# Performance work log

Measured on AMD Instinct MI355X. Metric: run time of the kernel, lower is better.

The kernel has to match this reference:

```python
import jax, jax.numpy as jnp
import numpy as np

IN_FEATURES = 64 * 64 * 3  # 12288, hard-coded in the torch module

# Sign with straight-through estimator (BinaryNet-style): fwd = sign(x),
# bwd = grad * 1{|x| <= 1} (hardtanh clip).
@jax.custom_vjp
def ste_sign(x):
    return jnp.sign(x)

def _ste_fwd(x):
    return jnp.sign(x), x

def _ste_bwd(x, g):
    return (g * (jnp.abs(x) <= 1.0).astype(g.dtype),)

ste_sign.defvjp(_ste_fwd, _ste_bwd)


def setup_inputs() -> dict:
    key = jax.random.key(0)
    k1, k2 = jax.random.split(key)
    B, C = 8192, 1000
    inp = jax.random.normal(k1, (B, IN_FEATURES), dtype=jnp.float32)
    # Linear weight init scale ~ U(-1/sqrt(fan_in), 1/sqrt(fan_in)); use scaled normal
    weight = jax.random.normal(k2, (C, IN_FEATURES), dtype=jnp.float32) * (1.0 / np.sqrt(IN_FEATURES))
    return {"input": inp, "weight": weight}


def reference(input, weight):
    x = input.reshape(-1, IN_FEATURES)
    # F.linear(sign(x), sign(W)) = sign(x) @ sign(W)^T  -> [B, num_classes]
    return jnp.einsum("bd,cd->bc", ste_sign(x), ste_sign(weight))
```

## Files before the change

kernel.cpp:

```cpp
#include <hip/hip_runtime.h>
#include <hip/hip_bf16.h>


#define K_DIM   12288
#define N_CLS   1000
#define N_PAD   1024
#define KSPLIT  4
#define K_QUART (K_DIM / KSPLIT)
#define STAGE_BYTES (N_PAD * 64)
#define N_STAGE_TOT (K_DIM / 64)
#define CHUNK_STAGES 2
#define CHUNK_K  (CHUNK_STAGES * 64)
#define CHUNKS   (K_QUART / CHUNK_K)
#define M_TILE   64
#define B_ROWS   8192
#define WS_W_BYTES ((size_t)N_STAGE_TOT * STAGE_BYTES)
#define WS_P_BYTES ((size_t)B_ROWS * N_CLS * 2 * KSPLIT)

typedef int int4v __attribute__((ext_vector_type(4)));
typedef unsigned int uint4v __attribute__((ext_vector_type(4)));

__device__ __forceinline__ unsigned sign_byte(unsigned bits) {
    unsigned mag = bits & 0x7fffffffu;
    unsigned nz = mag ? 1u : 0u;
    int sgn = ((int)bits) >> 31;
    int v = (((int)nz) ^ sgn) - sgn;
    return (unsigned)(v & 0xff);
}

__device__ __forceinline__ unsigned pack4(uint4v b) {
    return sign_byte(b.x) | (sign_byte(b.y) << 8) |
           (sign_byte(b.z) << 16) | (sign_byte(b.w) << 24);
}

__global__ void pack_w_kernel(const float* __restrict__ w,
                              unsigned char* __restrict__ ws) {
    const int gid = blockIdx.x * 256 + threadIdx.x;
    const int stage = gid >> 12;
    const int n = (gid >> 2) & 1023;
    const int q16 = gid & 3;
    const int k = stage * 64 + q16 * 16;
    uint4v o = {0u, 0u, 0u, 0u};
    if (n < N_CLS) {
        const float* p = w + (size_t)n * K_DIM + k;
        o.x = pack4(*reinterpret_cast<const uint4v*>(p));
        o.y = pack4(*reinterpret_cast<const uint4v*>(p + 4));
        o.z = pack4(*reinterpret_cast<const uint4v*>(p + 8));
        o.w = pack4(*reinterpret_cast<const uint4v*>(p + 12));
    }
    *reinterpret_cast<uint4v*>(ws + (size_t)stage * STAGE_BYTES + n * 64 + q16 * 16) = o;
}

__global__ void zero_kernel(float* __restrict__ out) {
    const int i = blockIdx.x * 256 + threadIdx.x;
    float4 z = {0.f, 0.f, 0.f, 0.f};
    *reinterpret_cast<float4*>(out + (size_t)i * 4) = z;
}

__global__ void reduce_kernel(const unsigned* __restrict__ part,
                              float* __restrict__ out) {
    const int i = blockIdx.x * 256 + threadIdx.x;
    uint4v w0 = *reinterpret_cast<const uint4v*>(part + (size_t)i * 8);
    uint4v w1 = *reinterpret_cast<const uint4v*>(part + (size_t)i * 8 + 4);
    float4 f;
    f.x = (float)((int)(short)(w0.x & 0xffffu) + (int)(short)(w0.x >> 16)
                + (int)(short)(w0.y & 0xffffu) + (int)(short)(w0.y >> 16));
    f.y = (float)((int)(short)(w0.z & 0xffffu) + (int)(short)(w0.z >> 16)
                + (int)(short)(w0.w & 0xffffu) + (int)(short)(w0.w >> 16));
    f.z = (float)((int)(short)(w1.x & 0xffffu) + (int)(short)(w1.x >> 16)
                + (int)(short)(w1.y & 0xffffu) + (int)(short)(w1.y >> 16));
    f.w = (float)((int)(short)(w1.z & 0xffffu) + (int)(short)(w1.z >> 16)
                + (int)(short)(w1.w & 0xffffu) + (int)(short)(w1.w >> 16));
    *reinterpret_cast<float4*>(out + (size_t)i * 4) = f;
}

template<int USE_PARTIAL>
__global__ __launch_bounds__(512, 2)
void bgemm_kernel(const float* __restrict__ x,
                  const unsigned char* __restrict__ wq,
                  unsigned* __restrict__ part,
                  float* __restrict__ out) {
    __shared__ unsigned x_lds[2][M_TILE * 32];

    const int tid  = threadIdx.x;
    const int wave = tid >> 6;
    const int lane = tid & 63;
    const int q    = lane >> 4;
    const int l15  = lane & 15;
    const int bx   = blockIdx.x;
    const int mtile = bx >> 2;
    const int kh    = bx & 3;
    const int m0    = mtile * M_TILE;
    const int nbase = wave * 128;

    int4v acc[4][8];
#pragma unroll
    for (int i = 0; i < 4; ++i)
#pragma unroll
        for (int j = 0; j < 8; ++j)
            acc[i][j] = (int4v){0, 0, 0, 0};

    const int srow = tid >> 3;
    const int scol = tid & 7;
    const float* xp = x + (size_t)(m0 + srow) * K_DIM + kh * K_QUART + scol * 4;
    const int sw_w = (srow & 3) * 8;

    const unsigned char* wqb = wq + (size_t)(kh * (N_STAGE_TOT / KSPLIT)) * STAGE_BYTES
                               + (nbase + l15) * 64 + q * 16;
    const int rsw = (l15 & 3) * 8;

    uint4v xr[4];
#pragma unroll
    for (int i = 0; i < 4; ++i)
        xr[i] = __builtin_nontemporal_load(reinterpret_cast<const uint4v*>(xp + i * 32));
#pragma unroll
    for (int i = 0; i < 4; ++i)
        x_lds[0][srow * 32 + (((i * 8 + scol)) ^ sw_w)] = pack4(xr[i]);
    __syncthreads();

#pragma unroll 2
    for (int c = 0; c < CHUNKS; ++c) {
        const int cur = c & 1;
        if (c + 1 < CHUNKS) {
            const float* xpc = xp + (size_t)(c + 1) * CHUNK_K;
#pragma unroll
            for (int i = 0; i < 4; ++i)
                xr[i] = __builtin_nontemporal_load(reinterpret_cast<const uint4v*>(xpc + i * 32));
        }
        const unsigned char* wpc = wqb + (size_t)(c * CHUNK_STAGES) * STAGE_BYTES;
#pragma unroll
        for (int st = 0; st < CHUNK_STAGES; ++st) {
            int4v a[4];
#pragma unroll
            for (int mt = 0; mt < 4; ++mt)
                a[mt] = *reinterpret_cast<const int4v*>(
                    &x_lds[cur][(mt * 16 + l15) * 32 + ((st * 16 + q * 4) ^ rsw)]);
            const unsigned char* wp = wpc + st * STAGE_BYTES;
#pragma unroll
            for (int nt = 0; nt < 8; ++nt) {
                int4v b = *reinterpret_cast<const int4v*>(wp + nt * 1024);
#pragma unroll
                for (int mt = 0; mt < 4; ++mt)
                    acc[mt][nt] = __builtin_amdgcn_mfma_i32_16x16x64_i8(a[mt], b, acc[mt][nt], 0, 0, 0);
            }
        }
        if (c + 1 < CHUNKS) {
#pragma unroll
            for (int i = 0; i < 4; ++i)
                x_lds[cur ^ 1][srow * 32 + (((i * 8 + scol)) ^ sw_w)] = pack4(xr[i]);
        }
        __syncthreads();
    }

#pragma unroll
    for (int mt = 0; mt < 4; ++mt) {
#pragma unroll
        for (int nt = 0; nt < 8; ++nt) {
            const int col = nbase + nt * 16 + l15;
            if (col < N_CLS) {
#pragma unroll
                for (int r = 0; r < 4; ++r) {
                    const int row = m0 + mt * 16 + q * 4 + r;
                    const size_t idx = (size_t)row * N_CLS + col;
                    if (USE_PARTIAL) {
                        reinterpret_cast<short*>(part)[idx * 4 + kh] = (short)acc[mt][nt][r];
                    } else {
                        atomicAdd(&out[idx], (float)acc[mt][nt][r]);
                    }
                }
            }
        }
    }
}

extern "C" void kernel_launch(void* const* d_in, const int* in_sizes, int n_in,
                              void* d_out, int out_size, void* d_ws, size_t ws_size,
                              hipStream_t stream) {
    const float* x = (const float*)d_in[0];
    const float* w = (const float*)d_in[1];
    float* out = (float*)d_out;
    unsigned char* ws = (unsigned char*)d_ws;

    pack_w_kernel<<<3072, 256, 0, stream>>>(w, ws);

    unsigned* part = reinterpret_cast<unsigned*>(ws + WS_W_BYTES);
    const bool use_part = ws_size >= WS_W_BYTES + WS_P_BYTES;
    if (use_part) {
        bgemm_kernel<1><<<512, 512, 0, stream>>>(x, ws, part, out);
        reduce_kernel<<<(B_ROWS * N_CLS) / (4 * 256), 256, 0, stream>>>(part, out);
    } else {
        zero_kernel<<<(B_ROWS * N_CLS) / (4 * 256), 256, 0, stream>>>(out);
        bgemm_kernel<0><<<512, 512, 0, stream>>>(x, ws, part, out);
    }
}
```

Before: 702.5 us.

## Prefetch weight fragments into registers and store partials as planar k-split arrays

The main GEMM loop now loads the next stage's weight fragments into registers before the MFMAs that use the current ones, so global weight loads overlap with compute. Partial sums move from interleaved 4-short groups to one contiguous plane per k-split. That makes the epilogue stores land in a single plane and lets the reduce kernel read four planes with aligned vector loads. The launch-bound occupancy hint is raised from 2 to 4 blocks per CU, which with 512-thread blocks and large accumulator arrays may force register spills.

```diff
diff --git a/kernel.cpp b/kernel.cpp
--- a/kernel.cpp
+++ b/kernel.cpp
@@ -14,11 +14,13 @@
 #define CHUNKS   (K_QUART / CHUNK_K)
 #define M_TILE   64
 #define B_ROWS   8192
+#define PLANE    ((size_t)B_ROWS * N_CLS)
 #define WS_W_BYTES ((size_t)N_STAGE_TOT * STAGE_BYTES)
-#define WS_P_BYTES ((size_t)B_ROWS * N_CLS * 2 * KSPLIT)
+#define WS_P_BYTES (PLANE * 2 * KSPLIT)
 
 typedef int int4v __attribute__((ext_vector_type(4)));
 typedef unsigned int uint4v __attribute__((ext_vector_type(4)));
+typedef short short4v __attribute__((ext_vector_type(4)));
 
 __device__ __forceinline__ unsigned sign_byte(unsigned bits) {
     unsigned mag = bits & 0x7fffffffu;
@@ -57,28 +59,26 @@
     *reinterpret_cast<float4*>(out + (size_t)i * 4) = z;
 }
 
-__global__ void reduce_kernel(const unsigned* __restrict__ part,
+__global__ void reduce_kernel(const short* __restrict__ part,
                               float* __restrict__ out) {
-    const int i = blockIdx.x * 256 + threadIdx.x;
-    uint4v w0 = *reinterpret_cast<const uint4v*>(part + (size_t)i * 8);
-    uint4v w1 = *reinterpret_cast<const uint4v*>(part + (size_t)i * 8 + 4);
+    const size_t base = ((size_t)blockIdx.x * 256 + threadIdx.x) * 4;
+    short4v p0 = *reinterpret_cast<const short4v*>(part + base);
+    short4v p1 = *reinterpret_cast<const short4v*>(part + PLANE + base);
+    short4v p2 = *reinterpret_cast<const short4v*>(part + 2 * PLANE + base);
+    short4v p3 = *reinterpret_cast<const short4v*>(part + 3 * PLANE + base);
     float4 f;
-    f.x = (float)((int)(short)(w0.x & 0xffffu) + (int)(short)(w0.x >> 16)
-                + (int)(short)(w0.y & 0xffffu) + (int)(short)(w0.y >> 16));
-    f.y = (float)((int)(short)(w0.z & 0xffffu) + (int)(short)(w0.z >> 16)
-                + (int)(short)(w0.w & 0xffffu) + (int)(short)(w0.w >> 16));
-    f.z = (float)((int)(short)(w1.x & 0xffffu) + (int)(short)(w1.x >> 16)
-                + (int)(short)(w1.y & 0xffffu) + (int)(short)(w1.y >> 16));
-    f.w = (float)((int)(short)(w1.z & 0xffffu) + (int)(short)(w1.z >> 16)
-                + (int)(short)(w1.w & 0xffffu) + (int)(short)(w1.w >> 16));
-    *reinterpret_cast<float4*>(out + (size_t)i * 4) = f;
+    f.x = (float)((int)p0.x + (int)p1.x + (int)p2.x + (int)p3.x);
+    f.y = (float)((int)p0.y + (int)p1.y + (int)p2.y + (int)p3.y);
+    f.z = (float)((int)p0.z + (int)p1.z + (int)p2.z + (int)p3.z);
+    f.w = (float)((int)p0.w + (int)p1.w + (int)p2.w + (int)p3.w);
+    *reinterpret_cast<float4*>(out + base) = f;
 }
 
 template<int USE_PARTIAL>
-__global__ __launch_bounds__(512, 2)
+__global__ __launch_bounds__(512, 4)
 void bgemm_kernel(const float* __restrict__ x,
                   const unsigned char* __restrict__ wq,
-                  unsigned* __restrict__ part,
+                  short* __restrict__ part,
                   float* __restrict__ out) {
     __shared__ unsigned x_lds[2][M_TILE * 32];
 
@@ -116,34 +116,62 @@
 #pragma unroll
     for (int i = 0; i < 4; ++i)
         x_lds[0][srow * 32 + (((i * 8 + scol)) ^ sw_w)] = pack4(xr[i]);
+
+    int4v bpre[8];
+#pragma unroll
+    for (int nt = 0; nt < 8; ++nt)
+        bpre[nt] = *reinterpret_cast<const int4v*>(wqb + nt * 1024);
     __syncthreads();
 
 #pragma unroll 2
     for (int c = 0; c < CHUNKS; ++c) {
         const int cur = c & 1;
+        const unsigned char* wpc = wqb + (size_t)(c * CHUNK_STAGES) * STAGE_BYTES;
+
+        int4v b1[8];
+#pragma unroll
+        for (int nt = 0; nt < 8; ++nt)
+            b1[nt] = *reinterpret_cast<const int4v*>(wpc + STAGE_BYTES + nt * 1024);
         if (c + 1 < CHUNKS) {
             const float* xpc = xp + (size_t)(c + 1) * CHUNK_K;
 #pragma unroll
             for (int i = 0; i < 4; ++i)
                 xr[i] = __builtin_nontemporal_load(reinterpret_cast<const uint4v*>(xpc + i * 32));
         }
-        const unsigned char* wpc = wqb + (size_t)(c * CHUNK_STAGES) * STAGE_BYTES;
-#pragma unroll
-        for (int st = 0; st < CHUNK_STAGES; ++st) {
+
+        {
             int4v a[4];
 #pragma unroll
             for (int mt = 0; mt < 4; ++mt)
                 a[mt] = *reinterpret_cast<const int4v*>(
-                    &x_lds[cur][(mt * 16 + l15) * 32 + ((st * 16 + q * 4) ^ rsw)]);
-            const unsigned char* wp = wpc + st * STAGE_BYTES;
-#pragma unroll
-            for (int nt = 0; nt < 8; ++nt) {
-                int4v b = *reinterpret_cast<const int4v*>(wp + nt * 1024);
+                    &x_lds[cur][(mt * 16 + l15) * 32 + ((q * 4) ^ rsw)]);
+#pragma unroll
+            for (int nt = 0; nt < 8; ++nt)
 #pragma unroll
                 for (int mt = 0; mt < 4; ++mt)
-                    acc[mt][nt] = __builtin_amdgcn_mfma_i32_16x16x64_i8(a[mt], b, acc[mt][nt], 0, 0, 0);
-            }
-        }
+                    acc[mt][nt] = __builtin_amdgcn_mfma_i32_16x16x64_i8(a[mt], bpre[nt], acc[mt][nt], 0, 0, 0);
+        }
+
+        if (c + 1 < CHUNKS) {
+            const unsigned char* wpn = wqb + (size_t)((c + 1) * CHUNK_STAGES) * STAGE_BYTES;
+#pragma unroll
+            for (int nt = 0; nt < 8; ++nt)
+                bpre[nt] = *reinterpret_cast<const int4v*>(wpn + nt * 1024);
+        }
+
+        {
+            int4v a[4];
+#pragma unroll
+            for (int mt = 0; mt < 4; ++mt)
+                a[mt] = *reinterpret_cast<const int4v*>(
+                    &x_lds[cur][(mt * 16 + l15) * 32 + ((16 + q * 4) ^ rsw)]);
+#pragma unroll
+            for (int nt = 0; nt < 8; ++nt)
+#pragma unroll
+                for (int mt = 0; mt < 4; ++mt)
+                    acc[mt][nt] = __builtin_amdgcn_mfma_i32_16x16x64_i8(a[mt], b1[nt], acc[mt][nt], 0, 0, 0);
+        }
+
         if (c + 1 < CHUNKS) {
 #pragma unroll
             for (int i = 0; i < 4; ++i)
@@ -152,6 +180,7 @@
         __syncthreads();
     }
 
+    short* pplane = part + (size_t)kh * PLANE;
 #pragma unroll
     for (int mt = 0; mt < 4; ++mt) {
 #pragma unroll
@@ -163,7 +192,7 @@
                     const int row = m0 + mt * 16 + q * 4 + r;
                     const size_t idx = (size_t)row * N_CLS + col;
                     if (USE_PARTIAL) {
-                        reinterpret_cast<short*>(part)[idx * 4 + kh] = (short)acc[mt][nt][r];
+                        pplane[idx] = (short)acc[mt][nt][r];
                     } else {
                         atomicAdd(&out[idx], (float)acc[mt][nt][r]);
                     }
@@ -183,7 +212,7 @@
 
     pack_w_kernel<<<3072, 256, 0, stream>>>(w, ws);
 
-    unsigned* part = reinterpret_cast<unsigned*>(ws + WS_W_BYTES);
+    short* part = reinterpret_cast<short*>(ws + WS_W_BYTES);
     const bool use_part = ws_size >= WS_W_BYTES + WS_P_BYTES;
     if (use_part) {
         bgemm_kernel<1><<<512, 512, 0, stream>>>(x, ws, part, out);
```

After: 1.854 ms. +163.9%, slower.
